# Kernel tuning notes

Hardware: AMD Instinct MI355X
Metric: run time of the kernel (lower is better)

Reference implementation:

```python
import jax, jax.numpy as jnp
import numpy as np

B, K, D, H = 32768, 16, 256, 2
HD = D // H
LN_EPS = 1e-5


def setup_inputs() -> dict:
    key = jax.random.key(0)
    ks = jax.random.split(key, 10)
    s = 1.0 / np.sqrt(D)
    return {
        "center_emb": jax.random.normal(ks[0], (B, D), dtype=jnp.float32),
        "neighbor_embs": jax.random.normal(ks[1], (B, K, D), dtype=jnp.float32),
        "edge_weights": jax.random.uniform(ks[2], (B, K), dtype=jnp.float32),
        "Wq": jax.random.uniform(ks[3], (D, D), jnp.float32, -s, s),
        "Wk": jax.random.uniform(ks[4], (D, D), jnp.float32, -s, s),
        "Wv": jax.random.uniform(ks[5], (D, D), jnp.float32, -s, s),
        "Wc": jax.random.uniform(ks[6], (D // 2, D), jnp.float32, -s, s),
        "Wx": jax.random.uniform(ks[7], (D // 2, D), jnp.float32, -s, s),
        "ln_gamma": jnp.ones((D,), jnp.float32),
        "ln_beta": jnp.zeros((D,), jnp.float32),
    }


def reference(center_emb, neighbor_embs, edge_weights, Wq, Wk, Wv, Wc, Wx, ln_gamma, ln_beta):
    scale = HD ** -0.5
    # projections (nn.Linear: x @ W.T)
    q = (center_emb @ Wq.T).reshape(B, H, HD)          # [B,H,hd]
    k = (neighbor_embs @ Wk.T).reshape(B, K, H, HD)    # [B,K,H,hd]
    v = (neighbor_embs @ Wv.T).reshape(B, K, H, HD)
    # attention scores with additive edge-weight topology bias
    scores = jnp.einsum("bhd,bkhd->bhk", q, k) * scale + edge_weights[:, None, :]
    attn = jax.nn.softmax(scores, axis=-1)             # [B,H,K] (dropout: eval mode)
    context = jnp.einsum("bhk,bkhd->bhd", attn, v).reshape(B, D)
    # LayerNorm over D
    mu = jnp.mean(context, axis=-1, keepdims=True)
    var = jnp.var(context, axis=-1, keepdims=True)
    ctx_n = (context - mu) * jax.lax.rsqrt(var + LN_EPS) * ln_gamma + ln_beta
    # concat of center / context half-projections
    return jnp.concatenate([center_emb @ Wc.T, ctx_n @ Wx.T], axis=-1)
```

## Files before the change

kernel.cpp:

```cpp
#include <hip/hip_runtime.h>

#define Bsz 32768
#define BR  32
#define SCALE 0.08838834764831845f

typedef __attribute__((ext_vector_type(4))) float f32x4;
typedef __attribute__((ext_vector_type(4))) unsigned short us4;
typedef __attribute__((ext_vector_type(8))) unsigned short us8;
typedef __attribute__((ext_vector_type(4))) unsigned int ui4;
typedef __attribute__((ext_vector_type(2))) unsigned int ui2;
typedef _Float16 __attribute__((ext_vector_type(2))) h2;
typedef _Float16 __attribute__((ext_vector_type(8))) h8;

static __device__ __forceinline__ unsigned int pk16(float a, float b){
  return __builtin_bit_cast(unsigned int, __builtin_amdgcn_cvt_pkrtz(a, b));
}
static __device__ __forceinline__ h2 uph(unsigned int u){
  return __builtin_bit_cast(h2, u);
}
static __device__ __forceinline__ float h2f(unsigned short h){
  return (float)__builtin_bit_cast(_Float16, h);
}
static __device__ __forceinline__ unsigned short f16b(float x){
  return __builtin_bit_cast(unsigned short, (_Float16)x);
}
static __device__ __forceinline__ h8 ldh8(const unsigned short* p){
  return __builtin_bit_cast(h8, *(const us8*)p);
}
#define FDOT2(a, b, c) __builtin_amdgcn_fdot2((a), (b), (c), false)
#define MFMA16(a, b, c) __builtin_amdgcn_mfma_f32_16x16x32_f16((a), (b), (c), 0, 0, 0)

__global__ void prep_kernel(const float* __restrict__ Wq, const float* __restrict__ Wk,
                            const float* __restrict__ Wv, const float* __restrict__ Wc,
                            const float* __restrict__ Wx, unsigned int* __restrict__ wsp){
  unsigned int* W1P = wsp;
  unsigned int* W2P = wsp + 128*640;
  unsigned int* W3P = W2P + 128*256;
  unsigned short* W1M = (unsigned short*)(wsp + 131072);
  const int n = blockIdx.x;
  const int k = threadIdx.x;
  float val;
  if (n < 512){
    const int h = n >> 8, m = n & 255;
    const float* wq = Wq + h*128*256 + k;
    const float* wk = Wk + h*128*256 + m;
    float s = 0.f;
    for (int d = 0; d < 128; ++d) s += wq[d*256] * wk[d*256];
    val = s;
  } else if (n < 640){
    val = Wc[(n-512)*256 + k];
  } else if (n < 896){
    val = Wv[(n-640)*256 + k];
  } else {
    val = Wx[(n-896)*256 + k];
  }
  if (n >= 512 && n < 640) W1M[(n-512)*256 + k] = f16b(val);
  const float vo = __shfl_xor(val, 1, 64);
  if ((k & 1) == 0){
    const unsigned int p = pk16(val, vo);
    const int kp = k >> 1;
    if (n < 640)      W1P[kp*640 + n] = p;
    else if (n < 896) W2P[kp*256 + (n-640)] = p;
    else              W3P[kp*128 + (n-896)] = p;
  }
}

__global__ __launch_bounds__(256, 4) void fused_kernel(
    const float* __restrict__ center, const float* __restrict__ nbr,
    const float* __restrict__ ew, const float* __restrict__ gamma,
    const float* __restrict__ beta, const unsigned int* __restrict__ Wall,
    float* __restrict__ out)
{
  __shared__ __align__(16) unsigned short s_ctil[BR*520];

  const int tid  = threadIdx.x;
  const int wid  = tid >> 6;
  const int lane = tid & 63;
  const int b0   = blockIdx.x * BR;

  const unsigned int* W1P = Wall;
  const unsigned int* W2P = Wall + 128*640;
  const unsigned int* W3P = W2P + 128*256;
  const unsigned short* W1M = (const unsigned short*)(Wall + 131072);

  const int rt = tid >> 5;
  const int ct = tid & 31;

  {
    const int sr = tid >> 3;
    const int fc = (tid & 7) * 32;
    const float* cp = center + ((long)(b0 + sr) << 8) + fc;
    #pragma unroll
    for (int it = 0; it < 4; ++it){
      float4 a = *(const float4*)(cp + it*8);
      float4 b = *(const float4*)(cp + it*8 + 4);
      ui4 v = {pk16(a.x,a.y), pk16(a.z,a.w), pk16(b.x,b.y), pk16(b.z,b.w)};
      *(ui4*)&s_ctil[sr*520 + 256 + fc + it*8] = v;
    }
  }
  __syncthreads();

  {
    const int rowg = wid >> 1;
    const int colq = wid & 1;
    const int l15 = lane & 15, lq = lane >> 4;
    h8 af[8];
    #pragma unroll
    for (int kk = 0; kk < 8; ++kk)
      af[kk] = __builtin_bit_cast(h8,
        *(const us8*)&s_ctil[(rowg*16 + l15)*520 + 256 + kk*32 + lq*8]);
    f32x4 macc[4];
    #pragma unroll
    for (int t = 0; t < 4; ++t) macc[t] = (f32x4){0,0,0,0};
    #pragma unroll
    for (int kk = 0; kk < 8; ++kk)
      #pragma unroll
      for (int t = 0; t < 4; ++t){
        const int col = colq*64 + t*16 + l15;
        macc[t] = MFMA16(af[kk], ldh8(W1M + col*256 + kk*32 + lq*8), macc[t]);
      }
    #pragma unroll
    for (int t = 0; t < 4; ++t)
      #pragma unroll
      for (int j = 0; j < 4; ++j)
        out[((long)(b0 + rowg*16 + lq*4 + j) << 8) + colq*64 + t*16 + l15] = macc[t][j];
  }
  __syncthreads();

  {
    f32x4 acc[4][2];
    #pragma unroll
    for (int rr = 0; rr < 4; ++rr){ acc[rr][0] = (f32x4){0,0,0,0}; acc[rr][1] = (f32x4){0,0,0,0}; }
    #pragma unroll 1
    for (int k0 = 0; k0 < 256; k0 += 8){
      ui4 a8[4];
      #pragma unroll
      for (int rr = 0; rr < 4; ++rr)
        a8[rr] = *(const ui4*)&s_ctil[(4*rt+rr)*520 + 256 + k0];
      #pragma unroll
      for (int kp = 0; kp < 4; ++kp){
        const unsigned int* wrow = W1P + ((k0>>1) + kp)*640;
        const ui4 w0 = ((const ui4*)(wrow      ))[ct];
        const ui4 w1 = ((const ui4*)(wrow + 128))[ct];
        #pragma unroll
        for (int rr = 0; rr < 4; ++rr){
          const h2 a2 = uph(a8[rr][kp]);
          #pragma unroll
          for (int j = 0; j < 4; ++j){
            acc[rr][0][j] = FDOT2(a2, uph(w0[j]), acc[rr][0][j]);
            acc[rr][1][j] = FDOT2(a2, uph(w1[j]), acc[rr][1][j]);
          }
        }
      }
    }
    #pragma unroll
    for (int rr = 0; rr < 4; ++rr){
      const int r = 4*rt + rr;
      ui2 v0 = {pk16(acc[rr][0][0], acc[rr][0][1]), pk16(acc[rr][0][2], acc[rr][0][3])};
      ui2 v1 = {pk16(acc[rr][1][0], acc[rr][1][1]), pk16(acc[rr][1][2], acc[rr][1][3])};
      *(ui2*)&s_ctil[r*520 + ct*4]       = v0;
      *(ui2*)&s_ctil[r*520 + 128 + ct*4] = v1;
    }
  }

  {
    f32x4 acc[4][2];
    #pragma unroll
    for (int rr = 0; rr < 4; ++rr){ acc[rr][0] = (f32x4){0,0,0,0}; acc[rr][1] = (f32x4){0,0,0,0}; }
    #pragma unroll 1
    for (int k0 = 0; k0 < 256; k0 += 8){
      ui4 a8[4];
      #pragma unroll
      for (int rr = 0; rr < 4; ++rr)
        a8[rr] = *(const ui4*)&s_ctil[(4*rt+rr)*520 + 256 + k0];
      #pragma unroll
      for (int kp = 0; kp < 4; ++kp){
        const unsigned int* wrow = W1P + ((k0>>1) + kp)*640;
        const ui4 w2 = ((const ui4*)(wrow + 256))[ct];
        const ui4 w3 = ((const ui4*)(wrow + 384))[ct];
        #pragma unroll
        for (int rr = 0; rr < 4; ++rr){
          const h2 a2 = uph(a8[rr][kp]);
          #pragma unroll
          for (int j = 0; j < 4; ++j){
            acc[rr][0][j] = FDOT2(a2, uph(w2[j]), acc[rr][0][j]);
            acc[rr][1][j] = FDOT2(a2, uph(w3[j]), acc[rr][1][j]);
          }
        }
      }
    }
    #pragma unroll
    for (int rr = 0; rr < 4; ++rr){
      const int r = 4*rt + rr;
      ui2 v0 = {pk16(acc[rr][0][0], acc[rr][0][1]), pk16(acc[rr][0][2], acc[rr][0][3])};
      ui2 v1 = {pk16(acc[rr][1][0], acc[rr][1][1]), pk16(acc[rr][1][2], acc[rr][1][3])};
      *(ui2*)&s_ctil[r*520 + 256 + ct*4] = v0;
      *(ui2*)&s_ctil[r*520 + 384 + ct*4] = v1;
    }
  }

  {
    const int myk = ((lane>>4)&1)*8 + ((lane>>3)&1)*4 + ((lane>>2)&1)*2 + ((lane>>1)&1);
    const int myh = lane >> 5;
    #pragma unroll 1
    for (int rr = 0; rr < 8; ++rr){
      const int r = wid*8 + rr;
      const long b = b0 + r;
      float4 c0, c1;
      {
        us4 h0 = *(const us4*)&s_ctil[r*520 + lane*4];
        us4 h1 = *(const us4*)&s_ctil[r*520 + 256 + lane*4];
        c0.x=h2f(h0[0]); c0.y=h2f(h0[1]); c0.z=h2f(h0[2]); c0.w=h2f(h0[3]);
        c1.x=h2f(h1[0]); c1.y=h2f(h1[1]); c1.z=h2f(h1[2]); c1.w=h2f(h1[3]);
      }
      float4 xv[16];
      const float* npt = nbr + ((b << 4) << 8) + lane*4;
      #pragma unroll
      for (int k = 0; k < 16; ++k) xv[k] = *(const float4*)(npt + (k << 8));
      float P0[16], P1[16];
      #pragma unroll
      for (int k = 0; k < 16; ++k){
        P0[k] = xv[k].x*c0.x + xv[k].y*c0.y + xv[k].z*c0.z + xv[k].w*c0.w;
        P1[k] = xv[k].x*c1.x + xv[k].y*c1.y + xv[k].z*c1.z + xv[k].w*c1.w;
      }
      const int b5 = lane & 32, b4 = lane & 16, b3 = lane & 8, b2 = lane & 4, b1 = lane & 2;
      float Q[16];
      #pragma unroll
      for (int j = 0; j < 16; ++j){
        const float give = b5 ? P0[j] : P1[j];
        const float keep = b5 ? P1[j] : P0[j];
        Q[j] = keep + __shfl_xor(give, 32, 64);
      }
      float R[8];
      #pragma unroll
      for (int j = 0; j < 8; ++j){
        const float give = b4 ? Q[j] : Q[8+j];
        const float keep = b4 ? Q[8+j] : Q[j];
        R[j] = keep + __shfl_xor(give, 16, 64);
      }
      float S[4];
      #pragma unroll
      for (int j = 0; j < 4; ++j){
        const float give = b3 ? R[j] : R[4+j];
        const float keep = b3 ? R[4+j] : R[j];
        S[j] = keep + __shfl_xor(give, 8, 64);
      }
      float T[2];
      #pragma unroll
      for (int j = 0; j < 2; ++j){
        const float give = b2 ? S[j] : S[2+j];
        const float keep = b2 ? S[2+j] : S[j];
        T[j] = keep + __shfl_xor(give, 4, 64);
      }
      float U;
      {
        const float give = b1 ? T[0] : T[1];
        const float keep = b1 ? T[1] : T[0];
        U = keep + __shfl_xor(give, 2, 64);
      }
      const float sfull = U + __shfl_xor(U, 1, 64);
      const float erk = ew[b*16 + myk];
      const float e = __expf(sfull*SCALE + erk);
      float dn = e;
      dn += __shfl_xor(dn, 2, 64);
      dn += __shfl_xor(dn, 4, 64);
      dn += __shfl_xor(dn, 8, 64);
      dn += __shfl_xor(dn, 16, 64);
      const float w = e / dn;
      float* wbuf = (float*)&s_ctil[r*520 + 256];
      wbuf[myh*16 + myk] = w;
      f32x4 wv[8];
      #pragma unroll
      for (int t = 0; t < 8; ++t) wv[t] = ((const f32x4*)wbuf)[t];
      float4 agg0 = {0,0,0,0}, agg1 = {0,0,0,0};
      #pragma unroll
      for (int k = 0; k < 16; ++k){
        const float w0 = wv[k>>2][k&3];
        const float w1 = wv[4 + (k>>2)][k&3];
        agg0.x += w0*xv[k].x; agg0.y += w0*xv[k].y; agg0.z += w0*xv[k].z; agg0.w += w0*xv[k].w;
        agg1.x += w1*xv[k].x; agg1.y += w1*xv[k].y; agg1.z += w1*xv[k].z; agg1.w += w1*xv[k].w;
      }
      ui2 v0 = {pk16(agg0.x, agg0.y), pk16(agg0.z, agg0.w)};
      ui2 v1 = {pk16(agg1.x, agg1.y), pk16(agg1.z, agg1.w)};
      *(ui2*)&s_ctil[r*520 + lane*4]       = v0;
      *(ui2*)&s_ctil[r*520 + 256 + lane*4] = v1;
    }
  }

  {
    f32x4 cacc[4][2];
    #pragma unroll
    for (int rr = 0; rr < 4; ++rr){ cacc[rr][0] = (f32x4){0,0,0,0}; cacc[rr][1] = (f32x4){0,0,0,0}; }
    #pragma unroll 1
    for (int k0 = 0; k0 < 256; k0 += 8){
      ui4 a0[4], a1[4];
      #pragma unroll
      for (int rr = 0; rr < 4; ++rr){
        a0[rr] = *(const ui4*)&s_ctil[(4*rt+rr)*520 + k0];
        a1[rr] = *(const ui4*)&s_ctil[(4*rt+rr)*520 + 256 + k0];
      }
      #pragma unroll
      for (int kp = 0; kp < 4; ++kp){
        const unsigned int* wrow = W2P + ((k0>>1) + kp)*256;
        const ui4 w0 = ((const ui4*)(wrow      ))[ct];
        const ui4 w1 = ((const ui4*)(wrow + 128))[ct];
        #pragma unroll
        for (int rr = 0; rr < 4; ++rr){
          const h2 x0 = uph(a0[rr][kp]);
          const h2 x1 = uph(a1[rr][kp]);
          #pragma unroll
          for (int j = 0; j < 4; ++j){
            cacc[rr][0][j] = FDOT2(x0, uph(w0[j]), cacc[rr][0][j]);
            cacc[rr][1][j] = FDOT2(x1, uph(w1[j]), cacc[rr][1][j]);
          }
        }
      }
    }
    const f32x4 gv0 = ((const f32x4*)gamma)[ct], gv1 = ((const f32x4*)gamma)[32 + ct];
    const f32x4 bv0 = ((const f32x4*)beta )[ct], bv1 = ((const f32x4*)beta )[32 + ct];
    #pragma unroll
    for (int rr = 0; rr < 4; ++rr){
      float s = 0.f, q = 0.f;
      #pragma unroll
      for (int t = 0; t < 2; ++t)
        #pragma unroll
        for (int j = 0; j < 4; ++j){
          const float x = cacc[rr][t][j];
          s += x; q += x*x;
        }
      #pragma unroll
      for (int m = 16; m >= 1; m >>= 1){
        s += __shfl_xor(s, m, 64);
        q += __shfl_xor(q, m, 64);
      }
      const float mu  = s * (1.f/256.f);
      const float var = q * (1.f/256.f) - mu*mu;
      const float rs  = rsqrtf(var + 1e-5f);
      const int r = 4*rt + rr;
      float y0[4], y1[4];
      #pragma unroll
      for (int j = 0; j < 4; ++j){
        y0[j] = (cacc[rr][0][j] - mu)*rs*gv0[j] + bv0[j];
        y1[j] = (cacc[rr][1][j] - mu)*rs*gv1[j] + bv1[j];
      }
      ui2 v0 = {pk16(y0[0], y0[1]), pk16(y0[2], y0[3])};
      ui2 v1 = {pk16(y1[0], y1[1]), pk16(y1[2], y1[3])};
      *(ui2*)&s_ctil[r*520 + ct*4]       = v0;
      *(ui2*)&s_ctil[r*520 + 128 + ct*4] = v1;
    }
  }

  {
    f32x4 eacc[4];
    #pragma unroll
    for (int rr = 0; rr < 4; ++rr) eacc[rr] = (f32x4){0,0,0,0};
    #pragma unroll 1
    for (int k0 = 0; k0 < 256; k0 += 8){
      ui4 a8[4];
      #pragma unroll
      for (int rr = 0; rr < 4; ++rr)
        a8[rr] = *(const ui4*)&s_ctil[(4*rt+rr)*520 + k0];
      #pragma unroll
      for (int kp = 0; kp < 4; ++kp){
        const ui4 w = ((const ui4*)(W3P + ((k0>>1) + kp)*128))[ct];
        #pragma unroll
        for (int rr = 0; rr < 4; ++rr){
          const h2 x = uph(a8[rr][kp]);
          #pragma unroll
          for (int j = 0; j < 4; ++j)
            eacc[rr][j] = FDOT2(x, uph(w[j]), eacc[rr][j]);
        }
      }
    }
    #pragma unroll
    for (int rr = 0; rr < 4; ++rr)
      *(f32x4*)&out[((long)(b0 + 4*rt + rr) << 8) + 128 + ct*4] = eacc[rr];
  }
}

extern "C" void kernel_launch(void* const* d_in, const int* in_sizes, int n_in,
                              void* d_out, int out_size, void* d_ws, size_t ws_size,
                              hipStream_t stream){
  const float* center = (const float*)d_in[0];
  const float* nbr    = (const float*)d_in[1];
  const float* ew     = (const float*)d_in[2];
  const float* Wq     = (const float*)d_in[3];
  const float* Wk     = (const float*)d_in[4];
  const float* Wv     = (const float*)d_in[5];
  const float* Wc     = (const float*)d_in[6];
  const float* Wx     = (const float*)d_in[7];
  const float* gamma  = (const float*)d_in[8];
  const float* beta   = (const float*)d_in[9];
  (void)in_sizes; (void)n_in; (void)out_size;

  unsigned int* W = (unsigned int*)d_ws;
  (void)ws_size;

  prep_kernel<<<1024, 256, 0, stream>>>(Wq, Wk, Wv, Wc, Wx, W);
  fused_kernel<<<Bsz/BR, 256, 0, stream>>>(center, nbr, ew, gamma, beta, W, (float*)d_out);
}
```

Before: 252.4 us.

## Compute folded Q·K projection with MFMA alongside Wc in one fused GEMM

The prep kernel now stores all 640 rows of the first weight block (folded Wq·Wk per head plus Wc) as row-major fp16. The two scalar FDOT2 loops that built the 512-wide folded query are replaced by one MFMA GEMM over 40 column tiles, processed in groups of 5. Tiles below 32 are written as fp16 into shared memory, overwriting the center tile after a barrier, and the Wc tiles go straight to the output. This moves the largest per-block matmul from packed dot-product ALU work onto matrix cores. It also removes one pass and one layout, at the cost of more LDS writes with narrow scattered stores.

```diff
diff --git a/kernel.cpp b/kernel.cpp
--- a/kernel.cpp
+++ b/kernel.cpp
@@ -32,11 +32,10 @@
 
 __global__ void prep_kernel(const float* __restrict__ Wq, const float* __restrict__ Wk,
                             const float* __restrict__ Wv, const float* __restrict__ Wc,
-                            const float* __restrict__ Wx, unsigned int* __restrict__ wsp){
-  unsigned int* W1P = wsp;
-  unsigned int* W2P = wsp + 128*640;
-  unsigned int* W3P = W2P + 128*256;
-  unsigned short* W1M = (unsigned short*)(wsp + 131072);
+                            const float* __restrict__ Wx, unsigned short* __restrict__ wsp){
+  unsigned short* W1R = wsp;
+  unsigned int*   W2P = (unsigned int*)(wsp + 640*256);
+  unsigned int*   W3P = W2P + 128*256;
   const int n = blockIdx.x;
   const int k = threadIdx.x;
   float val;
@@ -54,21 +53,23 @@
   } else {
     val = Wx[(n-896)*256 + k];
   }
-  if (n >= 512 && n < 640) W1M[(n-512)*256 + k] = f16b(val);
-  const float vo = __shfl_xor(val, 1, 64);
-  if ((k & 1) == 0){
-    const unsigned int p = pk16(val, vo);
-    const int kp = k >> 1;
-    if (n < 640)      W1P[kp*640 + n] = p;
-    else if (n < 896) W2P[kp*256 + (n-640)] = p;
-    else              W3P[kp*128 + (n-896)] = p;
+  if (n < 640){
+    W1R[n*256 + k] = f16b(val);
+  } else {
+    const float vo = __shfl_xor(val, 1, 64);
+    if ((k & 1) == 0){
+      const unsigned int p = pk16(val, vo);
+      const int kp = k >> 1;
+      if (n < 896) W2P[kp*256 + (n-640)] = p;
+      else         W3P[kp*128 + (n-896)] = p;
+    }
   }
 }
 
 __global__ __launch_bounds__(256, 4) void fused_kernel(
     const float* __restrict__ center, const float* __restrict__ nbr,
     const float* __restrict__ ew, const float* __restrict__ gamma,
-    const float* __restrict__ beta, const unsigned int* __restrict__ Wall,
+    const float* __restrict__ beta, const unsigned short* __restrict__ Wall,
     float* __restrict__ out)
 {
   __shared__ __align__(16) unsigned short s_ctil[BR*520];
@@ -78,10 +79,9 @@
   const int lane = tid & 63;
   const int b0   = blockIdx.x * BR;
 
-  const unsigned int* W1P = Wall;
-  const unsigned int* W2P = Wall + 128*640;
-  const unsigned int* W3P = W2P + 128*256;
-  const unsigned short* W1M = (const unsigned short*)(Wall + 131072);
+  const unsigned short* W1R = Wall;
+  const unsigned int*   W2P = (const unsigned int*)(Wall + 640*256);
+  const unsigned int*   W3P = W2P + 128*256;
 
   const int rt = tid >> 5;
   const int ct = tid & 31;
@@ -102,102 +102,42 @@
 
   {
     const int rowg = wid >> 1;
-    const int colq = wid & 1;
+    const int colh = wid & 1;
     const int l15 = lane & 15, lq = lane >> 4;
     h8 af[8];
     #pragma unroll
     for (int kk = 0; kk < 8; ++kk)
       af[kk] = __builtin_bit_cast(h8,
         *(const us8*)&s_ctil[(rowg*16 + l15)*520 + 256 + kk*32 + lq*8]);
-    f32x4 macc[4];
-    #pragma unroll
-    for (int t = 0; t < 4; ++t) macc[t] = (f32x4){0,0,0,0};
-    #pragma unroll
-    for (int kk = 0; kk < 8; ++kk)
-      #pragma unroll
-      for (int t = 0; t < 4; ++t){
-        const int col = colq*64 + t*16 + l15;
-        macc[t] = MFMA16(af[kk], ldh8(W1M + col*256 + kk*32 + lq*8), macc[t]);
-      }
-    #pragma unroll
-    for (int t = 0; t < 4; ++t)
-      #pragma unroll
-      for (int j = 0; j < 4; ++j)
-        out[((long)(b0 + rowg*16 + lq*4 + j) << 8) + colq*64 + t*16 + l15] = macc[t][j];
+    __syncthreads();
+    #pragma unroll 1
+    for (int c0t = 0; c0t < 20; c0t += 5){
+      f32x4 acc[5];
+      #pragma unroll
+      for (int u = 0; u < 5; ++u) acc[u] = (f32x4){0,0,0,0};
+      #pragma unroll
+      for (int kk = 0; kk < 8; ++kk)
+        #pragma unroll
+        for (int u = 0; u < 5; ++u){
+          const int gt = colh*20 + c0t + u;
+          acc[u] = MFMA16(af[kk], ldh8(W1R + (gt*16 + l15)*256 + kk*32 + lq*8), acc[u]);
+        }
+      #pragma unroll
+      for (int u = 0; u < 5; ++u){
+        const int gt = colh*20 + c0t + u;
+        if (gt < 32){
+          #pragma unroll
+          for (int j = 0; j < 4; ++j)
+            s_ctil[(rowg*16 + lq*4 + j)*520 + gt*16 + l15] = f16b(acc[u][j]);
+        } else {
+          #pragma unroll
+          for (int j = 0; j < 4; ++j)
+            out[((long)(b0 + rowg*16 + lq*4 + j) << 8) + (gt-32)*16 + l15] = acc[u][j];
+        }
+      }
+    }
   }
   __syncthreads();
-
-  {
-    f32x4 acc[4][2];
-    #pragma unroll
-    for (int rr = 0; rr < 4; ++rr){ acc[rr][0] = (f32x4){0,0,0,0}; acc[rr][1] = (f32x4){0,0,0,0}; }
-    #pragma unroll 1
-    for (int k0 = 0; k0 < 256; k0 += 8){
-      ui4 a8[4];
-      #pragma unroll
-      for (int rr = 0; rr < 4; ++rr)
-        a8[rr] = *(const ui4*)&s_ctil[(4*rt+rr)*520 + 256 + k0];
-      #pragma unroll
-      for (int kp = 0; kp < 4; ++kp){
-        const unsigned int* wrow = W1P + ((k0>>1) + kp)*640;
-        const ui4 w0 = ((const ui4*)(wrow      ))[ct];
-        const ui4 w1 = ((const ui4*)(wrow + 128))[ct];
-        #pragma unroll
-        for (int rr = 0; rr < 4; ++rr){
-          const h2 a2 = uph(a8[rr][kp]);
-          #pragma unroll
-          for (int j = 0; j < 4; ++j){
-            acc[rr][0][j] = FDOT2(a2, uph(w0[j]), acc[rr][0][j]);
-            acc[rr][1][j] = FDOT2(a2, uph(w1[j]), acc[rr][1][j]);
-          }
-        }
-      }
-    }
-    #pragma unroll
-    for (int rr = 0; rr < 4; ++rr){
-      const int r = 4*rt + rr;
-      ui2 v0 = {pk16(acc[rr][0][0], acc[rr][0][1]), pk16(acc[rr][0][2], acc[rr][0][3])};
-      ui2 v1 = {pk16(acc[rr][1][0], acc[rr][1][1]), pk16(acc[rr][1][2], acc[rr][1][3])};
-      *(ui2*)&s_ctil[r*520 + ct*4]       = v0;
-      *(ui2*)&s_ctil[r*520 + 128 + ct*4] = v1;
-    }
-  }
-
-  {
-    f32x4 acc[4][2];
-    #pragma unroll
-    for (int rr = 0; rr < 4; ++rr){ acc[rr][0] = (f32x4){0,0,0,0}; acc[rr][1] = (f32x4){0,0,0,0}; }
-    #pragma unroll 1
-    for (int k0 = 0; k0 < 256; k0 += 8){
-      ui4 a8[4];
-      #pragma unroll
-      for (int rr = 0; rr < 4; ++rr)
-        a8[rr] = *(const ui4*)&s_ctil[(4*rt+rr)*520 + 256 + k0];
-      #pragma unroll
-      for (int kp = 0; kp < 4; ++kp){
-        const unsigned int* wrow = W1P + ((k0>>1) + kp)*640;
-        const ui4 w2 = ((const ui4*)(wrow + 256))[ct];
-        const ui4 w3 = ((const ui4*)(wrow + 384))[ct];
-        #pragma unroll
-        for (int rr = 0; rr < 4; ++rr){
-          const h2 a2 = uph(a8[rr][kp]);
-          #pragma unroll
-          for (int j = 0; j < 4; ++j){
-            acc[rr][0][j] = FDOT2(a2, uph(w2[j]), acc[rr][0][j]);
-            acc[rr][1][j] = FDOT2(a2, uph(w3[j]), acc[rr][1][j]);
-          }
-        }
-      }
-    }
-    #pragma unroll
-    for (int rr = 0; rr < 4; ++rr){
-      const int r = 4*rt + rr;
-      ui2 v0 = {pk16(acc[rr][0][0], acc[rr][0][1]), pk16(acc[rr][0][2], acc[rr][0][3])};
-      ui2 v1 = {pk16(acc[rr][1][0], acc[rr][1][1]), pk16(acc[rr][1][2], acc[rr][1][3])};
-      *(ui2*)&s_ctil[r*520 + 256 + ct*4] = v0;
-      *(ui2*)&s_ctil[r*520 + 384 + ct*4] = v1;
-    }
-  }
 
   {
     const int myk = ((lane>>4)&1)*8 + ((lane>>3)&1)*4 + ((lane>>2)&1)*2 + ((lane>>1)&1);
@@ -393,7 +333,7 @@
   const float* beta   = (const float*)d_in[9];
   (void)in_sizes; (void)n_in; (void)out_size;
 
-  unsigned int* W = (unsigned int*)d_ws;
+  unsigned short* W = (unsigned short*)d_ws;
   (void)ws_size;
 
   prep_kernel<<<1024, 256, 0, stream>>>(Wq, Wk, Wv, Wc, Wx, W);
```

New measurement: 219.3 us. -13.1%, faster.
